# Kernel optimization log

Hardware: AMD Instinct MI355X
Metric: run time of the kernel (lower is better)

Reference implementation:

```python
import jax, jax.numpy as jnp
import numpy as np

BLOCK_Q = 64
BLOCK_KV = 64
TOPK_RATIO = 0.125


def setup_inputs() -> dict:
    key = jax.random.key(0)
    k1, k2, k3 = jax.random.split(key, 3)
    B, H, L, D = 1, 16, 8192, 64
    q = jax.random.normal(k1, (B, H, L, D), dtype=jnp.float32)
    k = jax.random.normal(k2, (B, H, L, D), dtype=jnp.float32)
    v = jax.random.normal(k3, (B, H, L, D), dtype=jnp.float32)
    return {"q": q, "k": k, "v": v}


def _sparse_lut(q, k):
    # get_sparse_map: block mean-pool q and mean-centered k, score blocks, top-k key blocks
    B, H, L, D = q.shape
    Mb, Nb = L // BLOCK_Q, L // BLOCK_KV
    q_pool = q.reshape(B, H, Mb, BLOCK_Q, D).mean(axis=3)          # [B,H,Mb,D]
    smooth_k = k - k.mean(axis=-2, keepdims=True)
    k_pool = smooth_k.reshape(B, H, Nb, BLOCK_KV, D).mean(axis=3)  # [B,H,Nb,D]
    pred = jnp.einsum('bhmd,bhnd->bhmn', q_pool, k_pool)           # [B,H,Mb,Nb]
    topk = int(TOPK_RATIO * Nb)
    _, lut = jax.lax.top_k(pred, topk)                             # [B,H,Mb,topk]
    return lut


def reference(q, k, v):
    B, H, L, D = q.shape
    Mb, Nb = L // BLOCK_Q, L // BLOCK_KV
    lut = _sparse_lut(q, k)                                        # [B,H,Mb,T] int32
    T = lut.shape[-1]
    sm_scale = D ** -0.5

    kb = k.reshape(B, H, Nb, BLOCK_KV, D)
    vb = v.reshape(B, H, Nb, BLOCK_KV, D)
    bi = jnp.arange(B)[:, None, None, None]
    hi = jnp.arange(H)[None, :, None, None]
    # gather selected KV blocks per query block: [B,H,Mb,T,BLOCK_KV,D]
    k_sel = kb[bi, hi, lut].reshape(B, H, Mb, T * BLOCK_KV, D)
    v_sel = vb[bi, hi, lut].reshape(B, H, Mb, T * BLOCK_KV, D)

    qb = q.reshape(B, H, Mb, BLOCK_Q, D)
    s = jnp.einsum('bhmqd,bhmkd->bhmqk', qb, k_sel) * sm_scale     # [B,H,Mb,BQ,T*BKV]
    p = jax.nn.softmax(s, axis=-1)
    o = jnp.einsum('bhmqk,bhmkd->bhmqd', p, v_sel)
    return o.reshape(B, H, L, D)
```

## Files before the change

### kernel.cpp

```cpp
#include <hip/hip_runtime.h>
#include <hip/hip_bf16.h>


#define H_  16
#define L_  8192
#define D_  64
#define MB_ 128
#define NB_ 128
#define TK_ 16
#define ST_ 72

typedef __bf16 bf16x8 __attribute__((ext_vector_type(8)));
typedef __bf16 bf16x4 __attribute__((ext_vector_type(4)));
typedef short  s16x4  __attribute__((ext_vector_type(4)));
typedef float  f32x4  __attribute__((ext_vector_type(4)));
typedef unsigned short u16x8 __attribute__((ext_vector_type(8)));

union BFU { __hip_bfloat16 h; unsigned short u; };

static __device__ inline unsigned short f2bfu(float f) {
  BFU c; c.h = __float2bfloat16(f); return c.u;
}

static __device__ inline f32x4 mfma16(bf16x4 a, bf16x4 b, f32x4 c) {
#if __has_builtin(__builtin_amdgcn_mfma_f32_16x16x16bf16_1k)
  return __builtin_amdgcn_mfma_f32_16x16x16bf16_1k(
      __builtin_bit_cast(s16x4, a), __builtin_bit_cast(s16x4, b), c, 0, 0, 0);
#elif __has_builtin(__builtin_amdgcn_mfma_f32_16x16x16_bf16)
  return __builtin_amdgcn_mfma_f32_16x16x16_bf16(a, b, c, 0, 0, 0);
#else
  f32x4 d = c;
  asm("v_mfma_f32_16x16x16_bf16 %0, %1, %2, %0" : "+v"(d) : "v"(a), "v"(b));
  return d;
#endif
}

__device__ unsigned short g_qb[(size_t)H_ * L_ * D_];
__device__ unsigned short g_kb[(size_t)H_ * L_ * D_];
__device__ unsigned short g_vt[(size_t)H_ * D_ * L_];
__device__ float g_qpool[H_ * NB_ * 64];
__device__ float g_kpool[H_ * NB_ * 64];
__device__ int   g_lut[H_ * MB_ * TK_];

static __device__ inline void cvt8_2(const float4& f0, const float4& f1,
                                     unsigned short* dst) {
  u16x8 s;
  s[0] = f2bfu(f0.x); s[1] = f2bfu(f0.y); s[2] = f2bfu(f0.z); s[3] = f2bfu(f0.w);
  s[4] = f2bfu(f1.x); s[5] = f2bfu(f1.y); s[6] = f2bfu(f1.z); s[7] = f2bfu(f1.w);
  *(u16x8*)dst = s;
}

static __device__ inline void cvt8_2s(const float4& f0, const float4& f1,
                                      unsigned short* dst, float sc) {
  u16x8 s;
  s[0] = f2bfu(f0.x * sc); s[1] = f2bfu(f0.y * sc);
  s[2] = f2bfu(f0.z * sc); s[3] = f2bfu(f0.w * sc);
  s[4] = f2bfu(f1.x * sc); s[5] = f2bfu(f1.y * sc);
  s[6] = f2bfu(f1.z * sc); s[7] = f2bfu(f1.w * sc);
  *(u16x8*)dst = s;
}

__global__ __launch_bounds__(256)
void fusedpool_kernel(const float* __restrict__ q,
                      const float* __restrict__ k,
                      const float* __restrict__ v) {
  __shared__ float qt[64 * 64];
  __shared__ float kt[64 * 64];
  __shared__ __align__(16) unsigned short vt_s[64 * ST_];
  __shared__ float pq[4][64], pk[4][64];

  const int b = blockIdx.x;
  const int h = b >> 7, n = b & 127;
  const int t = threadIdx.x;
  const int r = t >> 2, c = (t & 3) * 16;
  const size_t base = (size_t)b * 4096 + r * 64 + c;
  const float cs = 0.18033688011112042f;

  float4 qf0 = *(const float4*)(q + base),      qf1 = *(const float4*)(q + base + 4);
  float4 qf2 = *(const float4*)(q + base + 8),  qf3 = *(const float4*)(q + base + 12);
  float4 kf0 = *(const float4*)(k + base),      kf1 = *(const float4*)(k + base + 4);
  float4 kf2 = *(const float4*)(k + base + 8),  kf3 = *(const float4*)(k + base + 12);
  float4 vf0 = *(const float4*)(v + base),      vf1 = *(const float4*)(v + base + 4);
  float4 vf2 = *(const float4*)(v + base + 8),  vf3 = *(const float4*)(v + base + 12);

  cvt8_2s(qf0, qf1, g_qb + base, cs);  cvt8_2s(qf2, qf3, g_qb + base + 8, cs);
  cvt8_2(kf0, kf1, g_kb + base);       cvt8_2(kf2, kf3, g_kb + base + 8);
  cvt8_2(vf0, vf1, vt_s + r * ST_ + c);
  cvt8_2(vf2, vf3, vt_s + r * ST_ + c + 8);

  *(float4*)(qt + r * 64 + c)      = qf0; *(float4*)(qt + r * 64 + c + 4)  = qf1;
  *(float4*)(qt + r * 64 + c + 8)  = qf2; *(float4*)(qt + r * 64 + c + 12) = qf3;
  *(float4*)(kt + r * 64 + c)      = kf0; *(float4*)(kt + r * 64 + c + 4)  = kf1;
  *(float4*)(kt + r * 64 + c + 8)  = kf2; *(float4*)(kt + r * 64 + c + 12) = kf3;
  __syncthreads();

  const int col = t & 63, g = t >> 6;
  float sq = 0.f, sk = 0.f;
  for (int rr = g * 16; rr < g * 16 + 16; ++rr) {
    sq += qt[rr * 64 + col];
    sk += kt[rr * 64 + col];
  }
  pq[g][col] = sq; pk[g][col] = sk;

  u16x8 va, vb;
  #pragma unroll
  for (int i = 0; i < 8; ++i) va[i] = vt_s[(c + i) * ST_ + r];
  #pragma unroll
  for (int i = 0; i < 8; ++i) vb[i] = vt_s[(c + 8 + i) * ST_ + r];
  const size_t vo = ((size_t)h * 64 + r) * (size_t)L_ + (size_t)n * 64 + c;
  *(u16x8*)(g_vt + vo)     = va;
  *(u16x8*)(g_vt + vo + 8) = vb;

  __syncthreads();
  if (t < 64) {
    g_qpool[b * 64 + t] = (pq[0][t] + pq[1][t] + pq[2][t] + pq[3][t]) * (1.f / 64.f);
    g_kpool[b * 64 + t] = (pk[0][t] + pk[1][t] + pk[2][t] + pk[3][t]) * (1.f / 64.f);
  }
}


__global__ void topk_kernel() {
  const int b = blockIdx.x;
  const int h = b >> 7;
  const int lane = threadIdx.x;
  const float4* qrow = (const float4*)(g_qpool + b * 64);
  const float4* k0 = (const float4*)(g_kpool + (h * NB_ + lane) * 64);
  const float4* k1 = (const float4*)(g_kpool + (h * NB_ + lane + 64) * 64);
  float v0 = 0.f, v1 = 0.f;
  for (int i = 0; i < 16; ++i) {
    float4 qv = qrow[i];
    float4 a = k0[i];
    float4 c = k1[i];
    v0 += qv.x * a.x + qv.y * a.y + qv.z * a.z + qv.w * a.w;
    v1 += qv.x * c.x + qv.y * c.y + qv.z * c.z + qv.w * c.w;
  }
  for (int t = 0; t < TK_; ++t) {
    float bv; int bi;
    if (v0 >= v1) { bv = v0; bi = lane; } else { bv = v1; bi = lane + 64; }
    for (int mask = 1; mask < 64; mask <<= 1) {
      float ov = __shfl_xor(bv, mask, 64);
      int   oi = __shfl_xor(bi, mask, 64);
      if (ov > bv || (ov == bv && oi < bi)) { bv = ov; bi = oi; }
    }
    if (lane == 0) g_lut[b * TK_ + t] = bi;
    if (bi == lane) v0 = -3.0e38f;
    else if (bi == lane + 64) v1 = -3.0e38f;
  }
}

__global__ __launch_bounds__(256, 3)
void attn_kernel(float* __restrict__ out) {
  __shared__ float LDSo[4][16][65];
  __shared__ float LDSr[4][64];

  const int blk = blockIdx.x;
  const int h = blk & 15, m = blk >> 4;
  const int t = threadIdx.x;
  const int w = t >> 6;
  const int lane = t & 63;
  const int l16 = lane & 15, quad = lane >> 4;

  const unsigned short* qg = g_qb + ((size_t)h * L_ + (size_t)m * 64) * D_;
  bf16x8 qb0[4], qb1[4];
  #pragma unroll
  for (int g = 0; g < 4; ++g) {
    const unsigned short* qp = qg + (16 * g + l16) * 64 + quad * 8;
    qb0[g] = *(const bf16x8*)(qp);
    qb1[g] = *(const bf16x8*)(qp + 32);
  }

  f32x4 o[4][4];
  #pragma unroll
  for (int n4 = 0; n4 < 4; ++n4)
    #pragma unroll
    for (int g = 0; g < 4; ++g) o[n4][g] = (f32x4){0.f, 0.f, 0.f, 0.f};
  float lsum[4] = {0.f, 0.f, 0.f, 0.f};

  const int* my_lut = g_lut + (h * MB_ + m) * TK_;
  const unsigned short* kh = g_kb + (size_t)h * L_ * D_;
  const unsigned short* vg = g_vt + (size_t)h * D_ * L_;
  const int krow = (16 * w + l16) * 64 + quad * 8;
  const int vcol = 16 * w + quad * 4;

  bf16x8 ka0[2], ka1[2];
  bf16x4 va[2][4];

  {
    const int kb0 = __builtin_amdgcn_readfirstlane(my_lut[0]);
    const unsigned short* kbp = kh + (size_t)kb0 * 4096 + krow;
    ka0[0] = *(const bf16x8*)(kbp);
    ka1[0] = *(const bf16x8*)(kbp + 32);
    const unsigned short* vbp = vg + (size_t)kb0 * 64 + vcol;
    #pragma unroll
    for (int n4 = 0; n4 < 4; ++n4)
      va[0][n4] = *(const bf16x4*)(vbp + (size_t)(16 * n4 + l16) * L_);
  }

  #pragma unroll
  for (int j = 0; j < TK_; ++j) {
    const int cb = j & 1, nb = cb ^ 1;
    if (j + 1 < TK_) {
      const int kbn = __builtin_amdgcn_readfirstlane(my_lut[j + 1]);
      const unsigned short* kbp = kh + (size_t)kbn * 4096 + krow;
      ka0[nb] = *(const bf16x8*)(kbp);
      ka1[nb] = *(const bf16x8*)(kbp + 32);
      const unsigned short* vbp = vg + (size_t)kbn * 64 + vcol;
      #pragma unroll
      for (int n4 = 0; n4 < 4; ++n4)
        va[nb][n4] = *(const bf16x4*)(vbp + (size_t)(16 * n4 + l16) * L_);
    }

    f32x4 acc[4];
    __builtin_amdgcn_s_setprio(1);
    #pragma unroll
    for (int g = 0; g < 4; ++g) {
      f32x4 z = (f32x4){0.f, 0.f, 0.f, 0.f};
      z = __builtin_amdgcn_mfma_f32_16x16x32_bf16(ka0[cb], qb0[g], z, 0, 0, 0);
      z = __builtin_amdgcn_mfma_f32_16x16x32_bf16(ka1[cb], qb1[g], z, 0, 0, 0);
      acc[g] = z;
    }
    __builtin_amdgcn_s_setprio(0);

    bf16x4 pb[4];
    #pragma unroll
    for (int g = 0; g < 4; ++g) {
      const float p0 = exp2f(acc[g][0]), p1 = exp2f(acc[g][1]);
      const float p2 = exp2f(acc[g][2]), p3 = exp2f(acc[g][3]);
      lsum[g] += (p0 + p1) + (p2 + p3);
      unsigned int d0, d1;
      asm("v_cvt_pk_bf16_f32 %0, %1, %2" : "=v"(d0) : "v"(p0), "v"(p1));
      asm("v_cvt_pk_bf16_f32 %0, %1, %2" : "=v"(d1) : "v"(p2), "v"(p3));
      uint2 dd; dd.x = d0; dd.y = d1;
      pb[g] = __builtin_bit_cast(bf16x4, dd);
    }

    __builtin_amdgcn_s_setprio(1);
    #pragma unroll
    for (int n4 = 0; n4 < 4; ++n4)
      #pragma unroll
      for (int g = 0; g < 4; ++g)
        o[n4][g] = mfma16(va[cb][n4], pb[g], o[n4][g]);
    __builtin_amdgcn_s_setprio(0);
  }

  #pragma unroll
  for (int g = 0; g < 4; ++g) {
    float rs = lsum[g];
    rs += __shfl_xor(rs, 16, 64);
    rs += __shfl_xor(rs, 32, 64);
    lsum[g] = rs;
  }
  if (quad == 0) {
    #pragma unroll
    for (int g = 0; g < 4; ++g) LDSr[w][16 * g + l16] = lsum[g];
  }
  __syncthreads();

  const int dr = t & 15, q0 = (t >> 4) * 4;
  float rinv[4];
  #pragma unroll
  for (int qq = 0; qq < 4; ++qq)
    rinv[qq] = 1.0f / (LDSr[0][q0 + qq] + LDSr[1][q0 + qq] +
                       LDSr[2][q0 + qq] + LDSr[3][q0 + qq]);

  const size_t obase = ((size_t)h * L_ + (size_t)m * 64) * D_;
  #pragma unroll
  for (int n4 = 0; n4 < 4; ++n4) {
    #pragma unroll
    for (int g = 0; g < 4; ++g)
      #pragma unroll
      for (int r = 0; r < 4; ++r)
        LDSo[w][quad * 4 + r][16 * g + l16] = o[n4][g][r];
    __syncthreads();
    #pragma unroll
    for (int qq = 0; qq < 4; ++qq) {
      const int qv = q0 + qq;
      const float s = LDSo[0][dr][qv] + LDSo[1][dr][qv] +
                      LDSo[2][dr][qv] + LDSo[3][dr][qv];
      out[obase + (size_t)qv * 64 + n4 * 16 + dr] = s * rinv[qq];
    }
    __syncthreads();
  }
}

extern "C" void kernel_launch(void* const* d_in, const int* in_sizes, int n_in,
                              void* d_out, int out_size, void* d_ws, size_t ws_size,
                              hipStream_t stream) {
  const float* q = (const float*)d_in[0];
  const float* k = (const float*)d_in[1];
  const float* v = (const float*)d_in[2];
  float* out = (float*)d_out;

  fusedpool_kernel<<<H_ * NB_, 256, 0, stream>>>(q, k, v);
  topk_kernel<<<H_ * MB_, 64, 0, stream>>>();
  attn_kernel<<<H_ * MB_, 256, 0, stream>>>(out);
}
```

Measured before the change: 266.4 us.

## Store K and V in MFMA fragment order for coalesced per-lane loads

```diff
diff --git a/kernel.cpp b/kernel.cpp
--- a/kernel.cpp
+++ b/kernel.cpp
@@ -35,9 +35,16 @@
 #endif
 }
 
+static __device__ inline bf16x4 lo4(bf16x8 v) {
+  return __builtin_shufflevector(v, v, 0, 1, 2, 3);
+}
+static __device__ inline bf16x4 hi4(bf16x8 v) {
+  return __builtin_shufflevector(v, v, 4, 5, 6, 7);
+}
+
 __device__ unsigned short g_qb[(size_t)H_ * L_ * D_];
-__device__ unsigned short g_kb[(size_t)H_ * L_ * D_];
-__device__ unsigned short g_vt[(size_t)H_ * D_ * L_];
+__device__ unsigned short g_kf[(size_t)H_ * NB_ * 4096];
+__device__ unsigned short g_vf[(size_t)H_ * NB_ * 4096];
 __device__ float g_qpool[H_ * NB_ * 64];
 __device__ float g_kpool[H_ * NB_ * 64];
 __device__ int   g_lut[H_ * MB_ * TK_];
@@ -70,7 +77,6 @@
   __shared__ float pq[4][64], pk[4][64];
 
   const int b = blockIdx.x;
-  const int h = b >> 7, n = b & 127;
   const int t = threadIdx.x;
   const int r = t >> 2, c = (t & 3) * 16;
   const size_t base = (size_t)b * 4096 + r * 64 + c;
@@ -84,7 +90,15 @@
   float4 vf2 = *(const float4*)(v + base + 8),  vf3 = *(const float4*)(v + base + 12);
 
   cvt8_2s(qf0, qf1, g_qb + base, cs);  cvt8_2s(qf2, qf3, g_qb + base + 8, cs);
-  cvt8_2(kf0, kf1, g_kb + base);       cvt8_2(kf2, kf3, g_kb + base + 8);
+
+  {
+    const int w_k = r >> 4, l16k = r & 15;
+    const int hf = c >> 5, quadA = (c & 31) >> 3;
+    unsigned short* kfp = g_kf + ((size_t)b * 4 + w_k) * 1024 + hf * 512 + l16k * 8;
+    cvt8_2(kf0, kf1, kfp + quadA * 128);
+    cvt8_2(kf2, kf3, kfp + (quadA + 1) * 128);
+  }
+
   cvt8_2(vf0, vf1, vt_s + r * ST_ + c);
   cvt8_2(vf2, vf3, vt_s + r * ST_ + c + 8);
 
@@ -102,14 +116,24 @@
   }
   pq[g][col] = sq; pk[g][col] = sk;
 
-  u16x8 va, vb;
-  #pragma unroll
-  for (int i = 0; i < 8; ++i) va[i] = vt_s[(c + i) * ST_ + r];
-  #pragma unroll
-  for (int i = 0; i < 8; ++i) vb[i] = vt_s[(c + 8 + i) * ST_ + r];
-  const size_t vo = ((size_t)h * 64 + r) * (size_t)L_ + (size_t)n * 64 + c;
-  *(u16x8*)(g_vt + vo)     = va;
-  *(u16x8*)(g_vt + vo + 8) = vb;
+  {
+    const int wv = t >> 6, lv = t & 63;
+    const int l16v = lv & 15, quadv = lv >> 4;
+    u16x8 f0, f1;
+    #pragma unroll
+    for (int n4 = 0; n4 < 2; ++n4)
+      #pragma unroll
+      for (int rr = 0; rr < 4; ++rr)
+        f0[n4 * 4 + rr] = vt_s[(16 * wv + quadv * 4 + rr) * ST_ + 16 * n4 + l16v];
+    #pragma unroll
+    for (int n4 = 2; n4 < 4; ++n4)
+      #pragma unroll
+      for (int rr = 0; rr < 4; ++rr)
+        f1[(n4 - 2) * 4 + rr] = vt_s[(16 * wv + quadv * 4 + rr) * ST_ + 16 * n4 + l16v];
+    unsigned short* vfp = g_vf + ((size_t)b * 4 + wv) * 1024 + lv * 16;
+    *(u16x8*)(vfp)     = f0;
+    *(u16x8*)(vfp + 8) = f1;
+  }
 
   __syncthreads();
   if (t < 64) {
@@ -153,8 +177,9 @@
   __shared__ float LDSo[4][16][65];
   __shared__ float LDSr[4][64];
 
-  const int blk = blockIdx.x;
-  const int h = blk & 15, m = blk >> 4;
+  const int flat = blockIdx.x;
+  const int h = (flat & 7) * 2 + ((flat >> 10) & 1);
+  const int m = (flat >> 3) & 127;
   const int t = threadIdx.x;
   const int w = t >> 6;
   const int lane = t & 63;
@@ -177,23 +202,17 @@
   float lsum[4] = {0.f, 0.f, 0.f, 0.f};
 
   const int* my_lut = g_lut + (h * MB_ + m) * TK_;
-  const unsigned short* kh = g_kb + (size_t)h * L_ * D_;
-  const unsigned short* vg = g_vt + (size_t)h * D_ * L_;
-  const int krow = (16 * w + l16) * 64 + quad * 8;
-  const int vcol = 16 * w + quad * 4;
-
-  bf16x8 ka0[2], ka1[2];
-  bf16x4 va[2][4];
+
+  bf16x8 ka0[2], ka1[2], vv01[2], vv23[2];
 
   {
     const int kb0 = __builtin_amdgcn_readfirstlane(my_lut[0]);
-    const unsigned short* kbp = kh + (size_t)kb0 * 4096 + krow;
-    ka0[0] = *(const bf16x8*)(kbp);
-    ka1[0] = *(const bf16x8*)(kbp + 32);
-    const unsigned short* vbp = vg + (size_t)kb0 * 64 + vcol;
-    #pragma unroll
-    for (int n4 = 0; n4 < 4; ++n4)
-      va[0][n4] = *(const bf16x4*)(vbp + (size_t)(16 * n4 + l16) * L_);
+    const unsigned short* kbp = g_kf + ((size_t)(h * NB_ + kb0) * 4 + w) * 1024;
+    ka0[0] = *(const bf16x8*)(kbp + lane * 8);
+    ka1[0] = *(const bf16x8*)(kbp + 512 + lane * 8);
+    const unsigned short* vbp = g_vf + ((size_t)(h * NB_ + kb0) * 4 + w) * 1024 + lane * 16;
+    vv01[0] = *(const bf16x8*)(vbp);
+    vv23[0] = *(const bf16x8*)(vbp + 8);
   }
 
   #pragma unroll
@@ -201,13 +220,12 @@
     const int cb = j & 1, nb = cb ^ 1;
     if (j + 1 < TK_) {
       const int kbn = __builtin_amdgcn_readfirstlane(my_lut[j + 1]);
-      const unsigned short* kbp = kh + (size_t)kbn * 4096 + krow;
-      ka0[nb] = *(const bf16x8*)(kbp);
-      ka1[nb] = *(const bf16x8*)(kbp + 32);
-      const unsigned short* vbp = vg + (size_t)kbn * 64 + vcol;
-      #pragma unroll
-      for (int n4 = 0; n4 < 4; ++n4)
-        va[nb][n4] = *(const bf16x4*)(vbp + (size_t)(16 * n4 + l16) * L_);
+      const unsigned short* kbp = g_kf + ((size_t)(h * NB_ + kbn) * 4 + w) * 1024;
+      ka0[nb] = *(const bf16x8*)(kbp + lane * 8);
+      ka1[nb] = *(const bf16x8*)(kbp + 512 + lane * 8);
+      const unsigned short* vbp = g_vf + ((size_t)(h * NB_ + kbn) * 4 + w) * 1024 + lane * 16;
+      vv01[nb] = *(const bf16x8*)(vbp);
+      vv23[nb] = *(const bf16x8*)(vbp + 8);
     }
 
     f32x4 acc[4];
@@ -234,12 +252,14 @@
       pb[g] = __builtin_bit_cast(bf16x4, dd);
     }
 
+    const bf16x4 va_[4] = { lo4(vv01[cb]), hi4(vv01[cb]),
+                            lo4(vv23[cb]), hi4(vv23[cb]) };
     __builtin_amdgcn_s_setprio(1);
     #pragma unroll
     for (int n4 = 0; n4 < 4; ++n4)
       #pragma unroll
       for (int g = 0; g < 4; ++g)
-        o[n4][g] = mfma16(va[cb][n4], pb[g], o[n4][g]);
+        o[n4][g] = mfma16(va_[n4], pb[g], o[n4][g]);
     __builtin_amdgcn_s_setprio(0);
   }
 
```

Result: faster. 221.5 us (-16.9%).
